# Kernel tuning notes

Measured on AMD Instinct MI355X. Metric: run time of the kernel, lower is better.

## Reference

```python
import jax, jax.numpy as jnp
import numpy as np
from jax import lax


def _conv(x, w, b):
    # x: [B, Cin, H, W], w: [Cout, Cin, 3, 3] -> [B, Cout, H, W] (SAME padding)
    y = lax.conv_general_dilated(x, w, (1, 1), 'SAME',
                                 dimension_numbers=('NCHW', 'OIHW', 'NCHW'))
    return y + b[None, :, None, None]


def _cell_step(h, c, x, w, b):
    gates = _conv(jnp.concatenate([x, h], axis=1), w, b)  # [B, 4, H, W]
    i, f, o, g = jnp.split(gates, 4, axis=1)
    c = jax.nn.sigmoid(f) * c + jax.nn.sigmoid(i) * jnp.tanh(g)
    h = jax.nn.sigmoid(o) * jnp.tanh(c)
    return h, c


def setup_inputs() -> dict:
    key = jax.random.key(0)
    k1, k2, k3 = jax.random.split(key, 3)
    T, B, C, H, W = 20, 1, 1, 1024, 1024
    data = jax.random.normal(k1, (T, B, C, H, W), dtype=jnp.float32)
    enc_w = jax.random.normal(k2, (4, 2, 3, 3), dtype=jnp.float32) * 0.3
    enc_b = jnp.zeros((4,), dtype=jnp.float32)
    dec_w = jax.random.normal(k3, (4, 2, 3, 3), dtype=jnp.float32) * 0.3
    dec_b = jnp.zeros((4,), dtype=jnp.float32)
    return {"data": data, "enc_w": enc_w, "enc_b": enc_b,
            "dec_w": dec_w, "dec_b": dec_b,
            "epoch": 0, "T_en": 20, "T_de": 20}


def reference(data, enc_w, enc_b, dec_w, dec_b, epoch, T_en, T_de):
    B, C, H, W = data.shape[1:]
    h0 = jnp.zeros((B, C, H, W), dtype=data.dtype)
    c0 = jnp.zeros((B, C, H, W), dtype=data.dtype)

    def enc_step(carry, x):
        h, c = _cell_step(carry[0], carry[1], x, enc_w, enc_b)
        return (h, c), None

    (h_enc, _), _ = lax.scan(enc_step, (h0, c0), data[epoch:T_en])

    # decoder_input = encoder_h[0][:, None, :, :] -> with B=C=1 this is h_enc itself
    dec_in = h_enc[0][:, None, :, :]  # [1, 1, H, W]

    def dec_step(carry, _):
        h, c = _cell_step(carry[0], carry[1], dec_in, dec_w, dec_b)
        return (h, c), None

    (h_dec, _), _ = lax.scan(dec_step, (h0, c0), None, length=T_de)
    return h_dec[0, 0]  # [H, W]
```

## Files before the change

kernel.cpp:

```cpp
#include <hip/hip_runtime.h>

#define W 1024
#define H 1024
#define PADX 16
#define PADY 8
#define XS 1056
#define YS 1040
#define FR ((size_t)XS * (size_t)YS)
#define NPIX (H * W)
#define TROWS 32
#define TCOLS 64
#define LRN 48
#define LCV 96
#define LCW 100
#define NSLOT 460
#define NB 512
#define LOG2E 1.4426950408889634f
#define TWOL  2.8853900817779268f

typedef float v2f __attribute__((ext_vector_type(2)));

__device__ __forceinline__ float frcp_(float v) { return __builtin_amdgcn_rcpf(v); }
__device__ __forceinline__ float exp2_(float v) { return __builtin_amdgcn_exp2f(v); }
__device__ __forceinline__ float sigm2_(float v)  { return frcp_(1.0f + exp2_(-v)); }
__device__ __forceinline__ float tanhg2_(float v) { return 1.0f - 2.0f * frcp_(1.0f + exp2_(v)); }
__device__ __forceinline__ float tanhc_(float v)  { return 1.0f - 2.0f * frcp_(1.0f + exp2_(TWOL * v)); }

__global__ __launch_bounds__(256) void init_ws(const float* __restrict__ ew,
                                               const float* __restrict__ eb,
                                               const float* __restrict__ dw,
                                               const float* __restrict__ db,
                                               float* __restrict__ ws) {
    const size_t n4 = 6 * (FR / 4);
    size_t i = (size_t)blockIdx.x * blockDim.x + threadIdx.x;
    const size_t stride = (size_t)gridDim.x * blockDim.x;
    float4* w4 = (float4*)ws;
    const float4 z = make_float4(0.f, 0.f, 0.f, 0.f);
    for (; i < n4; i += stride) w4[i] = z;
    if (blockIdx.x == 0) {
        float* wsc = ws + 6 * FR;
        const int t = threadIdx.x;
        if (t < 72)                   wsc[t] = ew[t] * ((t / 18 == 3) ? TWOL : LOG2E);
        else if (t < 76)              wsc[t] = eb[t - 72] * ((t - 72 == 3) ? TWOL : LOG2E);
        else if (t >= 80 && t < 152)  wsc[t] = dw[t - 80] * (((t - 80) / 18 == 3) ? TWOL : LOG2E);
        else if (t >= 152 && t < 156) wsc[t] = db[t - 152] * ((t - 152 == 3) ? TWOL : LOG2E);
    }
}

__device__ __forceinline__ void acc_row(float4 A, float4 Bq, float lm, float rp,
                                        const float* __restrict__ wg, int wofs, int dy,
                                        v2f acc[4][4]) {
    const v2f E0 = {A.x, A.y},   E1 = {A.z, A.w};
    const v2f E2 = {Bq.x, Bq.y}, E3 = {Bq.z, Bq.w};
    const v2f O0 = {lm, A.x},    O1 = {A.y, A.z};
    const v2f O2 = {A.w, Bq.x},  O3 = {Bq.y, Bq.z}, O4 = {Bq.w, rp};
#pragma unroll
    for (int co = 0; co < 4; ++co) {
        const float w0 = wg[co * 18 + wofs + dy * 3 + 0];
        const float w1 = wg[co * 18 + wofs + dy * 3 + 1];
        const float w2 = wg[co * 18 + wofs + dy * 3 + 2];
        const v2f W0 = {w0, w0}, W1 = {w1, w1}, W2 = {w2, w2};
        acc[co][0] += W0 * O0 + W1 * E0 + W2 * O1;
        acc[co][1] += W0 * O1 + W1 * E1 + W2 * O2;
        acc[co][2] += W0 * O2 + W1 * E2 + W2 * O3;
        acc[co][3] += W0 * O3 + W1 * E3 + W2 * O4;
    }
}

__device__ __forceinline__ void conv3x8_pk(const float* __restrict__ p, int stride,
                                           const float* __restrict__ wg, int wofs,
                                           v2f acc[4][4]) {
#pragma unroll
    for (int dy = 0; dy < 3; ++dy) {
        acc_row(*(const float4*)p, *(const float4*)(p + 4), p[-1], p[8], wg, wofs, dy, acc);
        p += stride;
    }
}

__device__ __forceinline__ void conv3x8_edge(const float* __restrict__ base, int gr, int gc0,
                                             const float* __restrict__ wg, int wofs,
                                             v2f acc[4][4]) {
    const bool colA = (unsigned)gc0 < (unsigned)W;
    const bool lmok = (unsigned)(gc0 - 1) < (unsigned)W;
    const bool rpok = (unsigned)(gc0 + 8) < (unsigned)W;
#pragma unroll
    for (int dy = 0; dy < 3; ++dy) {
        const int ry = gr - 1 + dy;
        const bool rok = (unsigned)ry < (unsigned)H;
        const float* row = base + (long)ry * W;
        float4 A = make_float4(0.f, 0.f, 0.f, 0.f);
        float4 Bq = make_float4(0.f, 0.f, 0.f, 0.f);
        float lm = 0.f, rp = 0.f;
        if (rok) {
            if (colA) { A = *(const float4*)(row + gc0); Bq = *(const float4*)(row + gc0 + 4); }
            if (lmok) lm = row[gc0 - 1];
            if (rpok) rp = row[gc0 + 8];
        }
        acc_row(A, Bq, lm, rp, wg, wofs, dy, acc);
    }
}

template<int NSTEPS, bool XC>
__global__ __launch_bounds__(NB)
__attribute__((amdgpu_waves_per_eu(4, 4)))
void fusedN(const float* __restrict__ xbase, size_t xstep,
            const float* __restrict__ hin, const float* __restrict__ cin,
            float* __restrict__ hout, float* __restrict__ cout_,
            const float* __restrict__ wg, const float* __restrict__ bg,
            float* __restrict__ dout, int zero_init)
{
    __shared__ float hT[2][LRN * LCW];
    const int tid = threadIdx.x;
    const int c0 = (blockIdx.x & 15) * TCOLS;
    const int r0 = (blockIdx.x >> 4) * TROWS;

    const bool has = tid < NSLOT;
    const int q   = tid / 10;
    const int jj  = tid - q * 10;
    const int lr  = 1 + q;
    const int lc  = 8 + 8 * jj;
    const int gr  = r0 - 8 + lr;
    const int gc0 = c0 - 8 + 8 * jj;
    const size_t gofs = (size_t)(gr + PADY) * XS + (gc0 + PADX);
    const bool inimg = ((unsigned)gr < (unsigned)H) && ((unsigned)gc0 < (unsigned)W);
    const bool safe = (r0 >= 8) && (r0 + 40 <= H) && (c0 >= 16) && (c0 + 80 <= W);

    for (int idx = tid; idx < LRN * (LCV / 4); idx += NB) {
        const int r = idx / (LCV / 4);
        const int k = idx - r * (LCV / 4);
        float4 v = make_float4(0.f, 0.f, 0.f, 0.f);
        if (!zero_init)
            v = *(const float4*)(hin + (size_t)(r0 + r) * XS + (c0 + 4 * k));
        *(float4*)(&hT[0][r * LCW + 4 * k]) = v;
        *(float4*)(&hT[1][r * LCW + 4 * k]) = make_float4(0.f, 0.f, 0.f, 0.f);
    }

    float cc[8];
    if (has && !zero_init) {
        const float4 a = *(const float4*)(cin + gofs);
        const float4 b = *(const float4*)(cin + gofs + 4);
        cc[0] = a.x; cc[1] = a.y; cc[2] = a.z; cc[3] = a.w;
        cc[4] = b.x; cc[5] = b.y; cc[6] = b.z; cc[7] = b.w;
    } else {
#pragma unroll
        for (int e = 0; e < 8; ++e) cc[e] = 0.f;
    }

    v2f xacc[4][4];
    if constexpr (XC) {
        if (has) {
#pragma unroll
            for (int co = 0; co < 4; ++co) {
                const v2f bb = {bg[co], bg[co]};
#pragma unroll
                for (int j = 0; j < 4; ++j) xacc[co][j] = bb;
            }
            conv3x8_pk(xbase + gofs - XS, XS, wg, 0, xacc);
        }
    }
    __syncthreads();

    float hh[8];
#pragma unroll
    for (int e = 0; e < 8; ++e) hh[e] = 0.f;

#pragma unroll
    for (int i = 1; i <= NSTEPS; ++i) {
        const float* hR = hT[(i + 1) & 1];
        float* hW       = hT[i & 1];
        const bool act = has && (lr >= i) && (lr < LRN - i);
        if (act) {
            v2f acc[4][4];
            if constexpr (XC) {
#pragma unroll
                for (int co = 0; co < 4; ++co)
#pragma unroll
                    for (int j = 0; j < 4; ++j) acc[co][j] = xacc[co][j];
            } else {
#pragma unroll
                for (int co = 0; co < 4; ++co) {
                    const v2f bb = {bg[co], bg[co]};
#pragma unroll
                    for (int j = 0; j < 4; ++j) acc[co][j] = bb;
                }
                const float* xp = xbase + (size_t)(i - 1) * xstep;
                if (safe)
                    conv3x8_pk(xp + (size_t)(gr - 1) * W + gc0, W, wg, 0, acc);
                else
                    conv3x8_edge(xp, gr, gc0, wg, 0, acc);
            }
            conv3x8_pk(hR + (lr - 1) * LCW + lc, LCW, wg, 9, acc);
#pragma unroll
            for (int jp = 0; jp < 4; ++jp) {
#pragma unroll
                for (int s = 0; s < 2; ++s) {
                    const int e = 2 * jp + s;
                    const float gi = sigm2_(acc[0][jp][s]);
                    const float gf = sigm2_(acc[1][jp][s]);
                    const float go = sigm2_(acc[2][jp][s]);
                    const float gg = tanhg2_(acc[3][jp][s]);
                    const float cn = gf * cc[e] + gi * gg;
                    cc[e] = cn;
                    hh[e] = inimg ? (go * tanhc_(cn)) : 0.f;
                }
            }
            *(float4*)(hW + lr * LCW + lc)     = make_float4(hh[0], hh[1], hh[2], hh[3]);
            *(float4*)(hW + lr * LCW + lc + 4) = make_float4(hh[4], hh[5], hh[6], hh[7]);
        }
        __syncthreads();
    }

    if (has && lr >= 8 && lr < 8 + TROWS && jj >= 1 && jj <= 8) {
        if (dout) {
            const size_t o = (size_t)gr * W + gc0;
            *(float4*)(dout + o)     = make_float4(hh[0], hh[1], hh[2], hh[3]);
            *(float4*)(dout + o + 4) = make_float4(hh[4], hh[5], hh[6], hh[7]);
        } else {
            *(float4*)(hout + gofs)      = make_float4(hh[0], hh[1], hh[2], hh[3]);
            *(float4*)(hout + gofs + 4)  = make_float4(hh[4], hh[5], hh[6], hh[7]);
            *(float4*)(cout_ + gofs)     = make_float4(cc[0], cc[1], cc[2], cc[3]);
            *(float4*)(cout_ + gofs + 4) = make_float4(cc[4], cc[5], cc[6], cc[7]);
        }
    }
}

extern "C" void kernel_launch(void* const* d_in, const int* in_sizes, int n_in,
                              void* d_out, int out_size, void* d_ws, size_t ws_size,
                              hipStream_t stream) {
    const float* data  = (const float*)d_in[0];
    const float* enc_w = (const float*)d_in[1];
    const float* enc_b = (const float*)d_in[2];
    const float* dec_w = (const float*)d_in[3];
    const float* dec_b = (const float*)d_in[4];

    float* ws  = (float*)d_ws;
    float* hE1 = ws + 0 * FR;
    float* cE1 = ws + 1 * FR;
    float* hE0 = ws + 2 * FR;
    float* cE0 = ws + 3 * FR;
    float* hX  = ws + 4 * FR;
    float* cX  = ws + 5 * FR;
    float* wsc = ws + 6 * FR;
    const float* encW = wsc;
    const float* encB = wsc + 72;
    const float* decW = wsc + 80;
    const float* decB = wsc + 152;
    float* dout = (float*)d_out;

    init_ws<<<2048, 256, 0, stream>>>(enc_w, enc_b, dec_w, dec_b, ws);

    dim3 blk(NB), grd(512);
    fusedN<8, false><<<grd, blk, 0, stream>>>(data,                    (size_t)NPIX,
                                              nullptr, nullptr, hE1, cE1, encW, encB, nullptr, 1);
    fusedN<8, false><<<grd, blk, 0, stream>>>(data + (size_t)8 * NPIX, (size_t)NPIX,
                                              hE1, cE1, hE0, cE0, encW, encB, nullptr, 0);
    fusedN<4, false><<<grd, blk, 0, stream>>>(data + (size_t)16 * NPIX, (size_t)NPIX,
                                              hE0, cE0, hE1, cE1, encW, encB, nullptr, 0);
    fusedN<8, true><<<grd, blk, 0, stream>>>(hE1, 0, nullptr, nullptr,
                                             hE0, cE0, decW, decB, nullptr, 1);
    fusedN<8, true><<<grd, blk, 0, stream>>>(hE1, 0, hE0, cE0,
                                             hX,  cX,  decW, decB, nullptr, 0);
    fusedN<4, true><<<grd, blk, 0, stream>>>(hE1, 0, hX,  cX,
                                             nullptr, nullptr, decW, decB, dout, 0);
}
```

Measured before the change: 350.2 us.

## Replace halo-recompute multi-launch scheme with persistent kernel using neighbor flag sync

The six launches, each recomputing an 8-row halo over 8 timesteps, become one persistent kernel in which each block owns a 32x64 tile for all 40 steps. After each step a block publishes its border h values to a global ring buffer and raises a flag, then waits only on its eight neighbors' flags before filling its LDS halo. This removes redundant halo computation and the global h/c round trips between launches. The cost is a spin-wait per step that depends on all 512 blocks being co-resident, with a spin cap that could silently give wrong results if it is hit.

```diff
diff --git a/kernel.cpp b/kernel.cpp
--- a/kernel.cpp
+++ b/kernel.cpp
@@ -2,19 +2,18 @@
 
 #define W 1024
 #define H 1024
-#define PADX 16
-#define PADY 8
-#define XS 1056
-#define YS 1040
-#define FR ((size_t)XS * (size_t)YS)
+#define TR 32
+#define TC 64
+#define NBX 16
+#define NBY 32
+#define NBLK (NBX * NBY)
+#define NT 512
+#define LST 72
+#define LROWS 34
+#define LBUF (LROWS * LST)
 #define NPIX (H * W)
-#define TROWS 32
-#define TCOLS 64
-#define LRN 48
-#define LCV 96
-#define LCW 100
-#define NSLOT 460
-#define NB 512
+#define BSTR 256
+#define SPIN_CAP 1000000
 #define LOG2E 1.4426950408889634f
 #define TWOL  2.8853900817779268f
 
@@ -26,202 +25,295 @@
 __device__ __forceinline__ float tanhg2_(float v) { return 1.0f - 2.0f * frcp_(1.0f + exp2_(v)); }
 __device__ __forceinline__ float tanhc_(float v)  { return 1.0f - 2.0f * frcp_(1.0f + exp2_(TWOL * v)); }
 
-__global__ __launch_bounds__(256) void init_ws(const float* __restrict__ ew,
-                                               const float* __restrict__ eb,
-                                               const float* __restrict__ dw,
-                                               const float* __restrict__ db,
-                                               float* __restrict__ ws) {
-    const size_t n4 = 6 * (FR / 4);
-    size_t i = (size_t)blockIdx.x * blockDim.x + threadIdx.x;
-    const size_t stride = (size_t)gridDim.x * blockDim.x;
-    float4* w4 = (float4*)ws;
-    const float4 z = make_float4(0.f, 0.f, 0.f, 0.f);
-    for (; i < n4; i += stride) w4[i] = z;
-    if (blockIdx.x == 0) {
-        float* wsc = ws + 6 * FR;
-        const int t = threadIdx.x;
-        if (t < 72)                   wsc[t] = ew[t] * ((t / 18 == 3) ? TWOL : LOG2E);
-        else if (t < 76)              wsc[t] = eb[t - 72] * ((t - 72 == 3) ? TWOL : LOG2E);
-        else if (t >= 80 && t < 152)  wsc[t] = dw[t - 80] * (((t - 80) / 18 == 3) ? TWOL : LOG2E);
-        else if (t >= 152 && t < 156) wsc[t] = db[t - 152] * ((t - 152 == 3) ? TWOL : LOG2E);
-    }
-}
-
-__device__ __forceinline__ void acc_row(float4 A, float4 Bq, float lm, float rp,
-                                        const float* __restrict__ wg, int wofs, int dy,
-                                        v2f acc[4][4]) {
-    const v2f E0 = {A.x, A.y},   E1 = {A.z, A.w};
-    const v2f E2 = {Bq.x, Bq.y}, E3 = {Bq.z, Bq.w};
-    const v2f O0 = {lm, A.x},    O1 = {A.y, A.z};
-    const v2f O2 = {A.w, Bq.x},  O3 = {Bq.y, Bq.z}, O4 = {Bq.w, rp};
+__global__ __launch_bounds__(NT) void init_ws(const float* __restrict__ ew,
+                                              const float* __restrict__ eb,
+                                              const float* __restrict__ dw,
+                                              const float* __restrict__ db,
+                                              int* __restrict__ flags,
+                                              float* __restrict__ wsc) {
+    const int t = threadIdx.x;
+    if (t < NBLK) flags[t] = 0;
+    if (t < 72)                   wsc[t] = ew[t] * ((t / 18 == 3) ? TWOL : LOG2E);
+    else if (t < 76)              wsc[t] = eb[t - 72] * ((t == 75) ? TWOL : LOG2E);
+    else if (t >= 80 && t < 152)  wsc[t] = dw[t - 80] * (((t - 80) / 18 == 3) ? TWOL : LOG2E);
+    else if (t >= 152 && t < 156) wsc[t] = db[t - 152] * ((t == 155) ? TWOL : LOG2E);
+}
+
+struct R6 { float lm; float4 m; float rp; };
+
+__device__ __forceinline__ R6 ld6(const float* __restrict__ p) {
+    R6 r; r.lm = p[-1]; r.m = *(const float4*)p; r.rp = p[4]; return r;
+}
+
+__device__ __forceinline__ R6 ldx_row(const float* __restrict__ fr, int ry, int cq) {
+    R6 r; r.m = make_float4(0.f, 0.f, 0.f, 0.f); r.lm = 0.f; r.rp = 0.f;
+    if ((unsigned)ry < (unsigned)H) {
+        const float* p = fr + (size_t)ry * W + cq;
+        r.m = *(const float4*)p;
+        if (cq > 0)     r.lm = p[-1];
+        if (cq + 4 < W) r.rp = p[4];
+    }
+    return r;
+}
+
+__device__ __forceinline__ void acc_row4(const R6& R, const float* __restrict__ wg,
+                                         int wofs, v2f acc[4][2]) {
+    const v2f E0 = {R.m.x, R.m.y}, E1 = {R.m.z, R.m.w};
+    const v2f O0 = {R.lm, R.m.x}, O1 = {R.m.y, R.m.z}, O2 = {R.m.w, R.rp};
 #pragma unroll
     for (int co = 0; co < 4; ++co) {
-        const float w0 = wg[co * 18 + wofs + dy * 3 + 0];
-        const float w1 = wg[co * 18 + wofs + dy * 3 + 1];
-        const float w2 = wg[co * 18 + wofs + dy * 3 + 2];
+        const float w0 = wg[co * 18 + wofs + 0];
+        const float w1 = wg[co * 18 + wofs + 1];
+        const float w2 = wg[co * 18 + wofs + 2];
         const v2f W0 = {w0, w0}, W1 = {w1, w1}, W2 = {w2, w2};
-        acc[co][0] += W0 * O0 + W1 * E0 + W2 * O1;
-        acc[co][1] += W0 * O1 + W1 * E1 + W2 * O2;
-        acc[co][2] += W0 * O2 + W1 * E2 + W2 * O3;
-        acc[co][3] += W0 * O3 + W1 * E3 + W2 * O4;
-    }
-}
-
-__device__ __forceinline__ void conv3x8_pk(const float* __restrict__ p, int stride,
-                                           const float* __restrict__ wg, int wofs,
-                                           v2f acc[4][4]) {
-#pragma unroll
-    for (int dy = 0; dy < 3; ++dy) {
-        acc_row(*(const float4*)p, *(const float4*)(p + 4), p[-1], p[8], wg, wofs, dy, acc);
-        p += stride;
-    }
-}
-
-__device__ __forceinline__ void conv3x8_edge(const float* __restrict__ base, int gr, int gc0,
-                                             const float* __restrict__ wg, int wofs,
-                                             v2f acc[4][4]) {
-    const bool colA = (unsigned)gc0 < (unsigned)W;
-    const bool lmok = (unsigned)(gc0 - 1) < (unsigned)W;
-    const bool rpok = (unsigned)(gc0 + 8) < (unsigned)W;
-#pragma unroll
-    for (int dy = 0; dy < 3; ++dy) {
-        const int ry = gr - 1 + dy;
-        const bool rok = (unsigned)ry < (unsigned)H;
-        const float* row = base + (long)ry * W;
-        float4 A = make_float4(0.f, 0.f, 0.f, 0.f);
-        float4 Bq = make_float4(0.f, 0.f, 0.f, 0.f);
-        float lm = 0.f, rp = 0.f;
-        if (rok) {
-            if (colA) { A = *(const float4*)(row + gc0); Bq = *(const float4*)(row + gc0 + 4); }
-            if (lmok) lm = row[gc0 - 1];
-            if (rpok) rp = row[gc0 + 8];
-        }
-        acc_row(A, Bq, lm, rp, wg, wofs, dy, acc);
-    }
-}
-
-template<int NSTEPS, bool XC>
-__global__ __launch_bounds__(NB)
+        acc[co][0] += W0 * O0; acc[co][0] += W1 * E0; acc[co][0] += W2 * O1;
+        acc[co][1] += W0 * O1; acc[co][1] += W1 * E1; acc[co][1] += W2 * O2;
+    }
+}
+
+template<bool BCAST>
+__device__ __forceinline__ void acc_row4_init(const R6& R, const float* __restrict__ wg,
+                                              int wofs, v2f acc[4][2],
+                                              const v2f* __restrict__ init) {
+    const v2f E0 = {R.m.x, R.m.y}, E1 = {R.m.z, R.m.w};
+    const v2f O0 = {R.lm, R.m.x}, O1 = {R.m.y, R.m.z}, O2 = {R.m.w, R.rp};
+#pragma unroll
+    for (int co = 0; co < 4; ++co) {
+        const float w0 = wg[co * 18 + wofs + 0];
+        const float w1 = wg[co * 18 + wofs + 1];
+        const float w2 = wg[co * 18 + wofs + 2];
+        const v2f W0 = {w0, w0}, W1 = {w1, w1}, W2 = {w2, w2};
+        const v2f b0 = BCAST ? init[co] : init[co * 2 + 0];
+        const v2f b1 = BCAST ? init[co] : init[co * 2 + 1];
+        acc[co][0] = W0 * O0 + b0; acc[co][0] += W1 * E0; acc[co][0] += W2 * O1;
+        acc[co][1] = W0 * O1 + b1; acc[co][1] += W1 * E1; acc[co][1] += W2 * O2;
+    }
+}
+
+__global__ __launch_bounds__(NT)
 __attribute__((amdgpu_waves_per_eu(4, 4)))
-void fusedN(const float* __restrict__ xbase, size_t xstep,
-            const float* __restrict__ hin, const float* __restrict__ cin,
-            float* __restrict__ hout, float* __restrict__ cout_,
-            const float* __restrict__ wg, const float* __restrict__ bg,
-            float* __restrict__ dout, int zero_init)
+void convlstm(const float* __restrict__ data,
+              int* __restrict__ flags,
+              float* __restrict__ bord,
+              const float* __restrict__ wsc,
+              float* __restrict__ dout)
 {
-    __shared__ float hT[2][LRN * LCW];
+    __shared__ float lds[2 * LBUF];
     const int tid = threadIdx.x;
-    const int c0 = (blockIdx.x & 15) * TCOLS;
-    const int r0 = (blockIdx.x >> 4) * TROWS;
-
-    const bool has = tid < NSLOT;
-    const int q   = tid / 10;
-    const int jj  = tid - q * 10;
-    const int lr  = 1 + q;
-    const int lc  = 8 + 8 * jj;
-    const int gr  = r0 - 8 + lr;
-    const int gc0 = c0 - 8 + 8 * jj;
-    const size_t gofs = (size_t)(gr + PADY) * XS + (gc0 + PADX);
-    const bool inimg = ((unsigned)gr < (unsigned)H) && ((unsigned)gc0 < (unsigned)W);
-    const bool safe = (r0 >= 8) && (r0 + 40 <= H) && (c0 >= 16) && (c0 + 80 <= W);
-
-    for (int idx = tid; idx < LRN * (LCV / 4); idx += NB) {
-        const int r = idx / (LCV / 4);
-        const int k = idx - r * (LCV / 4);
-        float4 v = make_float4(0.f, 0.f, 0.f, 0.f);
-        if (!zero_init)
-            v = *(const float4*)(hin + (size_t)(r0 + r) * XS + (c0 + 4 * k));
-        *(float4*)(&hT[0][r * LCW + 4 * k]) = v;
-        *(float4*)(&hT[1][r * LCW + 4 * k]) = make_float4(0.f, 0.f, 0.f, 0.f);
-    }
-
-    float cc[8];
-    if (has && !zero_init) {
-        const float4 a = *(const float4*)(cin + gofs);
-        const float4 b = *(const float4*)(cin + gofs + 4);
-        cc[0] = a.x; cc[1] = a.y; cc[2] = a.z; cc[3] = a.w;
-        cc[4] = b.x; cc[5] = b.y; cc[6] = b.z; cc[7] = b.w;
-    } else {
-#pragma unroll
-        for (int e = 0; e < 8; ++e) cc[e] = 0.f;
-    }
-
-    v2f xacc[4][4];
-    if constexpr (XC) {
-        if (has) {
-#pragma unroll
-            for (int co = 0; co < 4; ++co) {
-                const v2f bb = {bg[co], bg[co]};
-#pragma unroll
-                for (int j = 0; j < 4; ++j) xacc[co][j] = bb;
-            }
-            conv3x8_pk(xbase + gofs - XS, XS, wg, 0, xacc);
-        }
-    }
+    const int bid = blockIdx.x;
+    const int bx = bid & (NBX - 1), by = bid >> 4;
+    const int c0 = bx * TC, r0 = by * TR;
+    const int r = tid >> 4, g = tid & 15;
+    const int gr = r0 + r;
+    const int cq = c0 + 4 * g;
+
+    const float* wE = wsc;
+    const float* bE = wsc + 72;
+    const float* wD = wsc + 80;
+    const float* bD = wsc + 152;
+
+    const bool hNn = by > 0, hSn = by < NBY - 1, hWn = bx > 0, hEn = bx < NBX - 1;
+    const int nN = hNn ? bid - NBX : -1, nS = hSn ? bid + NBX : -1;
+    const int nWb = hWn ? bid - 1 : -1,  nEb = hEn ? bid + 1 : -1;
+    const int nNW = (hNn && hWn) ? bid - NBX - 1 : -1, nNE = (hNn && hEn) ? bid - NBX + 1 : -1;
+    const int nSW = (hSn && hWn) ? bid + NBX - 1 : -1, nSE = (hSn && hEn) ? bid + NBX + 1 : -1;
+
+    int csrc = -1, cidx = 0, cdst = 0;
+    const bool crew = tid < 196;
+    if (tid < 66) {
+        const int q = tid - 1;
+        cdst = 4 + q;
+        if (q < 0)       { csrc = nNW; cidx = 64 + 63; }
+        else if (q > 63) { csrc = nNE; cidx = 64 + 0; }
+        else             { csrc = nN;  cidx = 64 + q; }
+    } else if (tid < 132) {
+        const int q = tid - 67;
+        cdst = 33 * LST + 4 + q;
+        if (q < 0)       { csrc = nSW; cidx = 63; }
+        else if (q > 63) { csrc = nSE; cidx = 0; }
+        else             { csrc = nS;  cidx = q; }
+    } else if (tid < 164) {
+        const int rr = tid - 132;
+        cdst = (1 + rr) * LST + 3;  csrc = nWb; cidx = 160 + rr;
+    } else if (tid < 196) {
+        const int rr = tid - 164;
+        cdst = (1 + rr) * LST + 68; csrc = nEb; cidx = 128 + rr;
+    }
+
+    float4* l4 = (float4*)lds;
+#pragma unroll 1
+    for (int k = tid; k < LBUF / 4; k += NT) l4[k] = make_float4(0.f, 0.f, 0.f, 0.f);
+
+    v2f be[4], bd[4];
+#pragma unroll
+    for (int co = 0; co < 4; ++co) {
+        be[co] = (v2f){bE[co], bE[co]};
+        bd[co] = (v2f){bD[co], bD[co]};
+    }
+
+    float cc[4] = {0.f, 0.f, 0.f, 0.f};
+    float hh[4] = {0.f, 0.f, 0.f, 0.f};
+
+    R6 px0 = ldx_row(data, gr - 1, cq);
+    R6 px1 = ldx_row(data, gr,     cq);
+    R6 px2 = ldx_row(data, gr + 1, cq);
+
     __syncthreads();
 
-    float hh[8];
-#pragma unroll
-    for (int e = 0; e < 8; ++e) hh[e] = 0.f;
-
-#pragma unroll
-    for (int i = 1; i <= NSTEPS; ++i) {
-        const float* hR = hT[(i + 1) & 1];
-        float* hW       = hT[i & 1];
-        const bool act = has && (lr >= i) && (lr < LRN - i);
-        if (act) {
-            v2f acc[4][4];
-            if constexpr (XC) {
-#pragma unroll
-                for (int co = 0; co < 4; ++co)
-#pragma unroll
-                    for (int j = 0; j < 4; ++j) acc[co][j] = xacc[co][j];
-            } else {
-#pragma unroll
-                for (int co = 0; co < 4; ++co) {
-                    const v2f bb = {bg[co], bg[co]};
-#pragma unroll
-                    for (int j = 0; j < 4; ++j) acc[co][j] = bb;
+    int istep = 1, ib = 1;
+    const int hofs  = r * LST + 4 + 4 * g;
+    const int wofs_ = (1 + r) * LST + 4 + 4 * g;
+
+#pragma unroll 1
+    for (int d = 1; d <= 20; ++d) {
+        const float* hR = lds + ((d - 1) & 1) * LBUF;
+        float*       hW = lds + (d & 1) * LBUF;
+        v2f acc[4][2];
+        acc_row4_init<true>(px0, wE, 0, acc, be);
+        acc_row4(px1, wE, 3, acc);
+        acc_row4(px2, wE, 6, acc);
+        if (d < 20) {
+            const float* fr = data + (size_t)d * NPIX;
+            px0 = ldx_row(fr, gr - 1, cq);
+            px1 = ldx_row(fr, gr,     cq);
+            px2 = ldx_row(fr, gr + 1, cq);
+        }
+        {
+            const float* hp = hR + hofs;
+            const R6 h0 = ld6(hp), h1 = ld6(hp + LST), h2 = ld6(hp + 2 * LST);
+            acc_row4(h0, wE, 9, acc);
+            acc_row4(h1, wE, 12, acc);
+            acc_row4(h2, wE, 15, acc);
+        }
+#pragma unroll
+        for (int jp = 0; jp < 2; ++jp)
+#pragma unroll
+            for (int s = 0; s < 2; ++s) {
+                const int e = 2 * jp + s;
+                const float gi = sigm2_(acc[0][jp][s]);
+                const float gf = sigm2_(acc[1][jp][s]);
+                const float go = sigm2_(acc[2][jp][s]);
+                const float gg = tanhg2_(acc[3][jp][s]);
+                const float cn = gf * cc[e] + gi * gg;
+                cc[e] = cn;
+                hh[e] = go * tanhc_(cn);
+            }
+        *(float4*)(hW + wofs_) = make_float4(hh[0], hh[1], hh[2], hh[3]);
+        {
+            float* bp = bord + ((size_t)ib * NBLK + bid) * BSTR;
+            if (r == 0) {
+#pragma unroll
+                for (int s = 0; s < 4; ++s)
+                    __hip_atomic_store(bp + 4 * g + s, hh[s], __ATOMIC_RELAXED, __HIP_MEMORY_SCOPE_AGENT);
+            }
+            if (r == TR - 1) {
+#pragma unroll
+                for (int s = 0; s < 4; ++s)
+                    __hip_atomic_store(bp + 64 + 4 * g + s, hh[s], __ATOMIC_RELAXED, __HIP_MEMORY_SCOPE_AGENT);
+            }
+            if (g == 0)  __hip_atomic_store(bp + 128 + r, hh[0], __ATOMIC_RELAXED, __HIP_MEMORY_SCOPE_AGENT);
+            if (g == 15) __hip_atomic_store(bp + 160 + r, hh[3], __ATOMIC_RELAXED, __HIP_MEMORY_SCOPE_AGENT);
+        }
+        __syncthreads();
+        if (tid == 0)
+            __hip_atomic_store(flags + bid, istep, __ATOMIC_RELEASE, __HIP_MEMORY_SCOPE_AGENT);
+        if (crew) {
+            float v = 0.f;
+            if (csrc >= 0) {
+                int spins = 0;
+                while (__hip_atomic_load(flags + csrc, __ATOMIC_RELAXED, __HIP_MEMORY_SCOPE_AGENT) < istep) {
+                    __builtin_amdgcn_s_sleep(1);
+                    if (++spins > SPIN_CAP) break;
                 }
-                const float* xp = xbase + (size_t)(i - 1) * xstep;
-                if (safe)
-                    conv3x8_pk(xp + (size_t)(gr - 1) * W + gc0, W, wg, 0, acc);
-                else
-                    conv3x8_edge(xp, gr, gc0, wg, 0, acc);
-            }
-            conv3x8_pk(hR + (lr - 1) * LCW + lc, LCW, wg, 9, acc);
-#pragma unroll
-            for (int jp = 0; jp < 4; ++jp) {
-#pragma unroll
-                for (int s = 0; s < 2; ++s) {
-                    const int e = 2 * jp + s;
-                    const float gi = sigm2_(acc[0][jp][s]);
-                    const float gf = sigm2_(acc[1][jp][s]);
-                    const float go = sigm2_(acc[2][jp][s]);
-                    const float gg = tanhg2_(acc[3][jp][s]);
-                    const float cn = gf * cc[e] + gi * gg;
-                    cc[e] = cn;
-                    hh[e] = inimg ? (go * tanhc_(cn)) : 0.f;
+                __builtin_amdgcn_fence(__ATOMIC_ACQUIRE, "agent");
+                v = __hip_atomic_load(bord + ((size_t)ib * NBLK + csrc) * BSTR + cidx,
+                                      __ATOMIC_RELAXED, __HIP_MEMORY_SCOPE_AGENT);
+            }
+            hW[cdst] = v;
+        }
+        __syncthreads();
+        ++istep; ib = (ib == 2) ? 0 : ib + 1;
+    }
+
+    v2f xacc[4][2];
+    {
+        const float* hp = lds + hofs;
+        const R6 a0 = ld6(hp), a1 = ld6(hp + LST), a2 = ld6(hp + 2 * LST);
+        acc_row4_init<true>(a0, wD, 0, xacc, bd);
+        acc_row4(a1, wD, 3, xacc);
+        acc_row4(a2, wD, 6, xacc);
+    }
+    __syncthreads();
+#pragma unroll 1
+    for (int k = tid; k < LBUF / 4; k += NT) l4[k] = make_float4(0.f, 0.f, 0.f, 0.f);
+#pragma unroll
+    for (int e = 0; e < 4; ++e) cc[e] = 0.f;
+    __syncthreads();
+
+#pragma unroll 1
+    for (int d = 1; d <= 20; ++d) {
+        const float* hR = lds + ((istep - 1) & 1) * LBUF;
+        float*       hW = lds + (istep & 1) * LBUF;
+        v2f acc[4][2];
+        {
+            const float* hp = hR + hofs;
+            const R6 h0 = ld6(hp), h1 = ld6(hp + LST), h2 = ld6(hp + 2 * LST);
+            acc_row4_init<false>(h0, wD, 9, acc, &xacc[0][0]);
+            acc_row4(h1, wD, 12, acc);
+            acc_row4(h2, wD, 15, acc);
+        }
+#pragma unroll
+        for (int jp = 0; jp < 2; ++jp)
+#pragma unroll
+            for (int s = 0; s < 2; ++s) {
+                const int e = 2 * jp + s;
+                const float gi = sigm2_(acc[0][jp][s]);
+                const float gf = sigm2_(acc[1][jp][s]);
+                const float go = sigm2_(acc[2][jp][s]);
+                const float gg = tanhg2_(acc[3][jp][s]);
+                const float cn = gf * cc[e] + gi * gg;
+                cc[e] = cn;
+                hh[e] = go * tanhc_(cn);
+            }
+        if (d == 20) break;
+        *(float4*)(hW + wofs_) = make_float4(hh[0], hh[1], hh[2], hh[3]);
+        {
+            float* bp = bord + ((size_t)ib * NBLK + bid) * BSTR;
+            if (r == 0) {
+#pragma unroll
+                for (int s = 0; s < 4; ++s)
+                    __hip_atomic_store(bp + 4 * g + s, hh[s], __ATOMIC_RELAXED, __HIP_MEMORY_SCOPE_AGENT);
+            }
+            if (r == TR - 1) {
+#pragma unroll
+                for (int s = 0; s < 4; ++s)
+                    __hip_atomic_store(bp + 64 + 4 * g + s, hh[s], __ATOMIC_RELAXED, __HIP_MEMORY_SCOPE_AGENT);
+            }
+            if (g == 0)  __hip_atomic_store(bp + 128 + r, hh[0], __ATOMIC_RELAXED, __HIP_MEMORY_SCOPE_AGENT);
+            if (g == 15) __hip_atomic_store(bp + 160 + r, hh[3], __ATOMIC_RELAXED, __HIP_MEMORY_SCOPE_AGENT);
+        }
+        __syncthreads();
+        if (tid == 0)
+            __hip_atomic_store(flags + bid, istep, __ATOMIC_RELEASE, __HIP_MEMORY_SCOPE_AGENT);
+        if (crew) {
+            float v = 0.f;
+            if (csrc >= 0) {
+                int spins = 0;
+                while (__hip_atomic_load(flags + csrc, __ATOMIC_RELAXED, __HIP_MEMORY_SCOPE_AGENT) < istep) {
+                    __builtin_amdgcn_s_sleep(1);
+                    if (++spins > SPIN_CAP) break;
                 }
-            }
-            *(float4*)(hW + lr * LCW + lc)     = make_float4(hh[0], hh[1], hh[2], hh[3]);
-            *(float4*)(hW + lr * LCW + lc + 4) = make_float4(hh[4], hh[5], hh[6], hh[7]);
+                __builtin_amdgcn_fence(__ATOMIC_ACQUIRE, "agent");
+                v = __hip_atomic_load(bord + ((size_t)ib * NBLK + csrc) * BSTR + cidx,
+                                      __ATOMIC_RELAXED, __HIP_MEMORY_SCOPE_AGENT);
+            }
+            hW[cdst] = v;
         }
         __syncthreads();
-    }
-
-    if (has && lr >= 8 && lr < 8 + TROWS && jj >= 1 && jj <= 8) {
-        if (dout) {
-            const size_t o = (size_t)gr * W + gc0;
-            *(float4*)(dout + o)     = make_float4(hh[0], hh[1], hh[2], hh[3]);
-            *(float4*)(dout + o + 4) = make_float4(hh[4], hh[5], hh[6], hh[7]);
-        } else {
-            *(float4*)(hout + gofs)      = make_float4(hh[0], hh[1], hh[2], hh[3]);
-            *(float4*)(hout + gofs + 4)  = make_float4(hh[4], hh[5], hh[6], hh[7]);
-            *(float4*)(cout_ + gofs)     = make_float4(cc[0], cc[1], cc[2], cc[3]);
-            *(float4*)(cout_ + gofs + 4) = make_float4(cc[4], cc[5], cc[6], cc[7]);
-        }
-    }
+        ++istep; ib = (ib == 2) ? 0 : ib + 1;
+    }
+
+    *(float4*)(dout + (size_t)gr * W + cq) = make_float4(hh[0], hh[1], hh[2], hh[3]);
 }
 
 extern "C" void kernel_launch(void* const* d_in, const int* in_sizes, int n_in,
@@ -233,33 +325,12 @@
     const float* dec_w = (const float*)d_in[3];
     const float* dec_b = (const float*)d_in[4];
 
-    float* ws  = (float*)d_ws;
-    float* hE1 = ws + 0 * FR;
-    float* cE1 = ws + 1 * FR;
-    float* hE0 = ws + 2 * FR;
-    float* cE0 = ws + 3 * FR;
-    float* hX  = ws + 4 * FR;
-    float* cX  = ws + 5 * FR;
-    float* wsc = ws + 6 * FR;
-    const float* encW = wsc;
-    const float* encB = wsc + 72;
-    const float* decW = wsc + 80;
-    const float* decB = wsc + 152;
-    float* dout = (float*)d_out;
-
-    init_ws<<<2048, 256, 0, stream>>>(enc_w, enc_b, dec_w, dec_b, ws);
-
-    dim3 blk(NB), grd(512);
-    fusedN<8, false><<<grd, blk, 0, stream>>>(data,                    (size_t)NPIX,
-                                              nullptr, nullptr, hE1, cE1, encW, encB, nullptr, 1);
-    fusedN<8, false><<<grd, blk, 0, stream>>>(data + (size_t)8 * NPIX, (size_t)NPIX,
-                                              hE1, cE1, hE0, cE0, encW, encB, nullptr, 0);
-    fusedN<4, false><<<grd, blk, 0, stream>>>(data + (size_t)16 * NPIX, (size_t)NPIX,
-                                              hE0, cE0, hE1, cE1, encW, encB, nullptr, 0);
-    fusedN<8, true><<<grd, blk, 0, stream>>>(hE1, 0, nullptr, nullptr,
-                                             hE0, cE0, decW, decB, nullptr, 1);
-    fusedN<8, true><<<grd, blk, 0, stream>>>(hE1, 0, hE0, cE0,
-                                             hX,  cX,  decW, decB, nullptr, 0);
-    fusedN<4, true><<<grd, blk, 0, stream>>>(hE1, 0, hX,  cX,
-                                             nullptr, nullptr, decW, decB, dout, 0);
-}
+    float* ws    = (float*)d_ws;
+    int*   flags = (int*)ws;
+    float* bord  = ws + 512;
+    float* wsc   = bord + 3 * NBLK * BSTR;
+    float* dout  = (float*)d_out;
+
+    init_ws<<<1, NT, 0, stream>>>(enc_w, enc_b, dec_w, dec_b, flags, wsc);
+    convlstm<<<NBLK, NT, 0, stream>>>(data, flags, bord, wsc, dout);
+}
```

Result: slower. 1.113 ms (+217.7%).

## Zero only padding borders in init and merge LSTM gate reciprocals

Applied to the files above, without the earlier changes.

The workspace init now zeroes only the padded halo rows and columns of each of the six frames instead of clearing the whole buffers, because interior cells are always overwritten before they are read. The LSTM gate math is rewritten algebraically so the cell update and the output each need one reciprocal instead of several, cutting transcendental instructions per pixel. The combined products (1+E) terms can overflow to inf for large pre-activations, so saturation behaviour may differ slightly. The init grid is also shrunk to 512 blocks.

```diff
diff --git a/kernel.cpp b/kernel.cpp
--- a/kernel.cpp
+++ b/kernel.cpp
@@ -22,21 +22,26 @@
 
 __device__ __forceinline__ float frcp_(float v) { return __builtin_amdgcn_rcpf(v); }
 __device__ __forceinline__ float exp2_(float v) { return __builtin_amdgcn_exp2f(v); }
-__device__ __forceinline__ float sigm2_(float v)  { return frcp_(1.0f + exp2_(-v)); }
-__device__ __forceinline__ float tanhg2_(float v) { return 1.0f - 2.0f * frcp_(1.0f + exp2_(v)); }
-__device__ __forceinline__ float tanhc_(float v)  { return 1.0f - 2.0f * frcp_(1.0f + exp2_(TWOL * v)); }
 
 __global__ __launch_bounds__(256) void init_ws(const float* __restrict__ ew,
                                                const float* __restrict__ eb,
                                                const float* __restrict__ dw,
                                                const float* __restrict__ db,
                                                float* __restrict__ ws) {
-    const size_t n4 = 6 * (FR / 4);
-    size_t i = (size_t)blockIdx.x * blockDim.x + threadIdx.x;
-    const size_t stride = (size_t)gridDim.x * blockDim.x;
+    const int NBF = 12416;
     float4* w4 = (float4*)ws;
     const float4 z = make_float4(0.f, 0.f, 0.f, 0.f);
-    for (; i < n4; i += stride) w4[i] = z;
+    for (int i = blockIdx.x * 256 + threadIdx.x; i < 6 * NBF;
+         i += gridDim.x * 256) {
+        const int b = i / NBF;
+        const int j = i - b * NBF;
+        int r, c4;
+        if (j < 2112)      { r = j / 264;                    c4 = j - 264 * r; }
+        else if (j < 4224) { const int k = j - 2112; r = 1032 + k / 264; c4 = k % 264; }
+        else if (j < 8320) { const int k = j - 4224; r = 8 + (k >> 2);   c4 = k & 3; }
+        else               { const int k = j - 8320; r = 8 + (k >> 2);   c4 = 260 + (k & 3); }
+        w4[(size_t)b * (FR / 4) + (size_t)r * (XS / 4) + c4] = z;
+    }
     if (blockIdx.x == 0) {
         float* wsc = ws + 6 * FR;
         const int t = threadIdx.x;
@@ -50,10 +55,10 @@
 __device__ __forceinline__ void acc_row(float4 A, float4 Bq, float lm, float rp,
                                         const float* __restrict__ wg, int wofs, int dy,
                                         v2f acc[4][4]) {
-    const v2f E0 = {A.x, A.y},   E1 = {A.z, A.w};
+    const v2f E0 = {A.x, A.y},  E1 = {A.z, A.w};
     const v2f E2 = {Bq.x, Bq.y}, E3 = {Bq.z, Bq.w};
-    const v2f O0 = {lm, A.x},    O1 = {A.y, A.z};
-    const v2f O2 = {A.w, Bq.x},  O3 = {Bq.y, Bq.z}, O4 = {Bq.w, rp};
+    const v2f O0 = {lm, A.x},   O1 = {A.y, A.z};
+    const v2f O2 = {A.w, Bq.x}, O3 = {Bq.y, Bq.z}, O4 = {Bq.w, rp};
 #pragma unroll
     for (int co = 0; co < 4; ++co) {
         const float w0 = wg[co * 18 + wofs + dy * 3 + 0];
@@ -190,18 +195,23 @@
                     conv3x8_edge(xp, gr, gc0, wg, 0, acc);
             }
             conv3x8_pk(hR + (lr - 1) * LCW + lc, LCW, wg, 9, acc);
+
 #pragma unroll
             for (int jp = 0; jp < 4; ++jp) {
 #pragma unroll
                 for (int s = 0; s < 2; ++s) {
                     const int e = 2 * jp + s;
-                    const float gi = sigm2_(acc[0][jp][s]);
-                    const float gf = sigm2_(acc[1][jp][s]);
-                    const float go = sigm2_(acc[2][jp][s]);
-                    const float gg = tanhg2_(acc[3][jp][s]);
-                    const float cn = gf * cc[e] + gi * gg;
+                    const float Ei = exp2_(-acc[0][jp][s]);
+                    const float Ef = exp2_(-acc[1][jp][s]);
+                    const float Eo = exp2_(-acc[2][jp][s]);
+                    const float Eg = exp2_(acc[3][jp][s]);
+                    const float Pp = (1.f + Eg) * (1.f + Ei);
+                    const float Qq = 1.f + Ef;
+                    const float cn = (cc[e] * Pp + (Eg - 1.f) * Qq) * frcp_(Pp * Qq);
                     cc[e] = cn;
-                    hh[e] = inimg ? (go * tanhc_(cn)) : 0.f;
+                    const float Ec = exp2_(TWOL * cn);
+                    const float hv = (Ec - 1.f) * frcp_((1.f + Eo) * (1.f + Ec));
+                    hh[e] = inimg ? hv : 0.f;
                 }
             }
             *(float4*)(hW + lr * LCW + lc)     = make_float4(hh[0], hh[1], hh[2], hh[3]);
@@ -247,12 +257,12 @@
     const float* decB = wsc + 152;
     float* dout = (float*)d_out;
 
-    init_ws<<<2048, 256, 0, stream>>>(enc_w, enc_b, dec_w, dec_b, ws);
+    init_ws<<<512, 256, 0, stream>>>(enc_w, enc_b, dec_w, dec_b, ws);
 
     dim3 blk(NB), grd(512);
-    fusedN<8, false><<<grd, blk, 0, stream>>>(data,                    (size_t)NPIX,
+    fusedN<8, false><<<grd, blk, 0, stream>>>(data,                     (size_t)NPIX,
                                               nullptr, nullptr, hE1, cE1, encW, encB, nullptr, 1);
-    fusedN<8, false><<<grd, blk, 0, stream>>>(data + (size_t)8 * NPIX, (size_t)NPIX,
+    fusedN<8, false><<<grd, blk, 0, stream>>>(data + (size_t)8 * NPIX,  (size_t)NPIX,
                                               hE1, cE1, hE0, cE0, encW, encB, nullptr, 0);
     fusedN<4, false><<<grd, blk, 0, stream>>>(data + (size_t)16 * NPIX, (size_t)NPIX,
                                               hE0, cE0, hE1, cE1, encW, encB, nullptr, 0);
```

After: 338.2 us. 1.04x faster.
